# Performance work log

Hardware: AMD Instinct MI355X
Metric: run time of the kernel (lower is better)

The kernel has to match this reference:

```python
import jax, jax.numpy as jnp
import numpy as np

DIM = 128
DIM_HEAD = 32
HEADS = 4
EPS = 1e-12  # F.normalize eps


def _l2_normalize(t, axis=-1):
    # matches torch F.normalize(p=2): x / max(||x||, eps)
    n = jnp.sqrt(jnp.sum(t * t, axis=axis, keepdims=True))
    return t / jnp.maximum(n, EPS)


def _dwconv3x3(x_nhwc, k_hwio, c):
    # depthwise 3x3, stride 1, SAME padding, no bias
    return jax.lax.conv_general_dilated(
        x_nhwc, k_hwio, window_strides=(1, 1), padding='SAME',
        dimension_numbers=('NHWC', 'HWIO', 'NHWC'), feature_group_count=c)


def setup_inputs() -> dict:
    key = jax.random.key(0)
    ks = jax.random.split(key, 10)
    b, h, w = 4, 256, 256
    inner = DIM_HEAD * HEADS  # == DIM
    s = 0.02
    return {
        'x': jax.random.normal(ks[0], (b, h, w, DIM), jnp.float32),
        'illumination_feature': jax.random.uniform(ks[1], (b, h, w, inner), jnp.float32),
        'Wq': jax.random.normal(ks[2], (DIM, inner), jnp.float32) * s,  # stored (in,out)
        'Wk': jax.random.normal(ks[3], (DIM, inner), jnp.float32) * s,
        'Wv': jax.random.normal(ks[4], (DIM, inner), jnp.float32) * s,
        'rescale': jnp.ones((HEADS, 1, 1), jnp.float32),
        'Wp': jax.random.normal(ks[5], (inner, DIM), jnp.float32) * s,
        'bp': jnp.zeros((DIM,), jnp.float32),
        'pe_w1': jax.random.normal(ks[6], (3, 3, 1, DIM), jnp.float32) * s,  # HWIO depthwise
        'pe_w2': jax.random.normal(ks[7], (3, 3, 1, DIM), jnp.float32) * s,
    }


def reference(x, illumination_feature, Wq, Wk, Wv, rescale, Wp, bp, pe_w1, pe_w2):
    b, h, w, c = x.shape
    n = h * w
    heads = rescale.shape[0]
    xf = x.reshape(b, n, c)
    ilf = illumination_feature.reshape(b, n, -1)

    q_inp = xf @ Wq  # [b,n,heads*d]
    k_inp = xf @ Wk
    v_inp = xf @ Wv

    def to_heads(t):  # b n (h d) -> b h n d
        return t.reshape(b, n, heads, -1).transpose(0, 2, 1, 3)

    q = to_heads(q_inp)
    k = to_heads(k_inp)
    v = to_heads(v_inp) * to_heads(ilf)  # illumination gating

    # transpose to channel attention layout: b h d n
    q = q.transpose(0, 1, 3, 2)
    k = k.transpose(0, 1, 3, 2)
    v = v.transpose(0, 1, 3, 2)

    q = _l2_normalize(q, axis=-1)
    k = _l2_normalize(k, axis=-1)

    attn = jnp.einsum('bhdn,bhen->bhde', k, q) * rescale  # [b,h,d,d]
    attn = jax.nn.softmax(attn, axis=-1)
    out = jnp.einsum('bhde,bhen->bhdn', attn, v)  # [b,h,d,n]

    # b h d n -> b n (h d)
    out = out.transpose(0, 3, 1, 2).reshape(b, n, -1)
    x1 = (out @ Wp + bp).reshape(b, h, w, c)

    # positional branch: depthwise conv -> GELU -> depthwise conv on v_inp (NHWC)
    v_img = v_inp.reshape(b, h, w, -1)
    x2 = _dwconv3x3(v_img, pe_w1, c)
    x2 = jax.nn.gelu(x2, approximate=False)
    x2 = _dwconv3x3(x2, pe_w2, c)

    return x1 + x2
```

## Files before the change

### kernel.cpp

```cpp
#include <hip/hip_runtime.h>
#include <math.h>

#define B_ 4
#define C_ 128
#define H_ 256
#define W_ 256
#define NPIX (H_*W_)
#define HEADS_ 4

typedef unsigned int uint;
typedef unsigned short ushort;
typedef __attribute__((ext_vector_type(8))) __bf16 bf16x8;
typedef __attribute__((ext_vector_type(4))) float f32x4;

__device__ __forceinline__ ushort f2bf(float f){
    uint u = __builtin_bit_cast(uint, f);
    u += 0x7FFFu + ((u>>16)&1u);
    return (ushort)(u>>16);
}
__device__ __forceinline__ float bf2f(ushort h){
    uint u = ((uint)h)<<16;
    return __builtin_bit_cast(float, u);
}
__device__ __forceinline__ __bf16 f2bfv(float f){
    return __builtin_bit_cast(__bf16, f2bf(f));
}
__device__ __forceinline__ int swz3(int i){ return (i ^ (i>>3)) & 7; }

__global__ __launch_bounds__(512) void k12(const float* __restrict__ x, const float* __restrict__ Wv,
                                           float* __restrict__ S, ushort* __restrict__ vinp){
    __shared__ __align__(16) char smX[32768];
    __shared__ __align__(16) char smT[32768];
    int blk = blockIdx.x;
    int b = blk >> 7, chunk = blk & 127;
    long base = ((long)b*NPIX + (long)chunk*512) * C_;
    int t = threadIdx.x, lane = t & 63, w = t >> 6;
    int wm = w >> 2, wn = w & 3;
    int m0 = wm*64, n0 = wn*32;

    bf16x8 Bv[4][2];
    #pragma unroll
    for(int kk=0;kk<4;kk++){
        int kb = kk*32 + (lane>>4)*8;
        #pragma unroll
        for(int j=0;j<2;j++){
            int col = n0 + j*16 + (lane&15);
            bf16x8 v;
            #pragma unroll
            for(int jj=0;jj<8;jj++) v[jj] = f2bfv(Wv[(kb+jj)*C_ + col]);
            Bv[kk][j] = v;
        }
    }

    f32x4 acc_s[4][2];
    #pragma unroll
    for(int i=0;i<4;i++)
        #pragma unroll
        for(int j=0;j<2;j++) acc_s[i][j] = {0.f,0.f,0.f,0.f};

    for(int tile=0; tile<4; ++tile){
        {
            int rp = (t>>5)*2;
            int c0 = (t&31)*4;
            const float* xp = x + base + (long)tile*128*C_;
            #pragma unroll
            for(int p=0;p<4;p++){
                int r = p*32 + rp;
                float4 a0 = *(const float4*)(xp + r*C_ + c0);
                float4 a1 = *(const float4*)(xp + (r+1)*C_ + c0);
                ushort h0[4] = {f2bf(a0.x), f2bf(a0.y), f2bf(a0.z), f2bf(a0.w)};
                ushort h1[4] = {f2bf(a1.x), f2bf(a1.y), f2bf(a1.z), f2bf(a1.w)};
                uint2 pk0, pk1;
                pk0.x = (uint)h0[0] | ((uint)h0[1]<<16);
                pk0.y = (uint)h0[2] | ((uint)h0[3]<<16);
                pk1.x = (uint)h1[0] | ((uint)h1[1]<<16);
                pk1.y = (uint)h1[2] | ((uint)h1[3]<<16);
                *(uint2*)(smX + r*256     + ((2*c0) ^ (swz3(r)<<4)))   = pk0;
                *(uint2*)(smX + (r+1)*256 + ((2*c0) ^ (swz3(r+1)<<4))) = pk1;
                #pragma unroll
                for(int i=0;i<4;i++){
                    int ch = c0+i;
                    uint pk = (uint)h0[i] | ((uint)h1[i]<<16);
                    *(uint*)(smT + ch*256 + ((2*r) ^ (swz3(ch)<<4))) = pk;
                }
            }
        }
        __syncthreads();

        f32x4 acc_v[4][2];
        #pragma unroll
        for(int i=0;i<4;i++)
            #pragma unroll
            for(int j=0;j<2;j++) acc_v[i][j] = {0.f,0.f,0.f,0.f};

        #pragma unroll
        for(int kk=0;kk<4;kk++){
            int kb = kk*32 + (lane>>4)*8;
            bf16x8 A[4];
            #pragma unroll
            for(int i=0;i<4;i++){
                int r = m0 + i*16 + (lane&15);
                A[i] = *(const bf16x8*)(smX + r*256 + ((2*kb) ^ (swz3(r)<<4)));
            }
            #pragma unroll
            for(int i=0;i<4;i++)
                #pragma unroll
                for(int j=0;j<2;j++)
                    acc_v[i][j] = __builtin_amdgcn_mfma_f32_16x16x32_bf16(A[i], Bv[kk][j], acc_v[i][j], 0,0,0);
            bf16x8 As[4], Bs[2];
            #pragma unroll
            for(int i=0;i<4;i++){
                int ch = m0 + i*16 + (lane&15);
                As[i] = *(const bf16x8*)(smT + ch*256 + ((2*kb) ^ (swz3(ch)<<4)));
            }
            #pragma unroll
            for(int j=0;j<2;j++){
                int ch = n0 + j*16 + (lane&15);
                Bs[j] = *(const bf16x8*)(smT + ch*256 + ((2*kb) ^ (swz3(ch)<<4)));
            }
            #pragma unroll
            for(int i=0;i<4;i++)
                #pragma unroll
                for(int j=0;j<2;j++)
                    acc_s[i][j] = __builtin_amdgcn_mfma_f32_16x16x32_bf16(As[i], Bs[j], acc_s[i][j], 0,0,0);
        }
        __syncthreads();
        {
            int rq = (lane>>4)*4, cc = lane&15;
            #pragma unroll
            for(int i=0;i<4;i++)
                #pragma unroll
                for(int j=0;j<2;j++)
                    #pragma unroll
                    for(int rg=0;rg<4;rg++){
                        int row = m0 + i*16 + rq + rg;
                        int col = n0 + j*16 + cc;
                        *(ushort*)(smX + row*256 + ((2*col) ^ (swz3(row)<<4))) = f2bf(acc_v[i][j][rg]);
                    }
        }
        __syncthreads();
        {
            long off = base + (long)tile*128*C_;
            #pragma unroll
            for(int p=0;p<4;p++){
                int idx = p*512 + t;
                int row = idx >> 4, ub = idx & 15;
                uint4 d = *(const uint4*)(smX + row*256 + ((ub*16) ^ (swz3(row)<<4)));
                *(uint4*)(vinp + off + row*C_ + ub*8) = d;
            }
        }
        __syncthreads();
    }
    float* Sb = S + b*C_*C_;
    int rq = (lane>>4)*4, cc = lane&15;
    #pragma unroll
    for(int i=0;i<4;i++)
        #pragma unroll
        for(int j=0;j<2;j++)
            #pragma unroll
            for(int rg=0;rg<4;rg++){
                int row = m0 + i*16 + rq + rg;
                int col = n0 + j*16 + cc;
                atomicAdd(&Sb[row*C_ + col], acc_s[i][j][rg]);
            }
}

__global__ __launch_bounds__(256) void k3a(const float* __restrict__ S, const float* __restrict__ Wq,
                                           const float* __restrict__ Wk, float* __restrict__ TQ,
                                           float* __restrict__ nrm){
    int b = blockIdx.x >> 7, c = blockIdx.x & 127;
    __shared__ float sS[C_];
    int t = threadIdx.x;
    if(t < C_) sS[t] = S[(b*C_+c)*C_ + t];
    __syncthreads();
    const float* Wm = (t < C_) ? Wq : Wk;
    int col = t & (C_-1);
    float acc = 0.f;
    #pragma unroll 4
    for(int c2=0;c2<C_;c2++) acc += sS[c2] * Wm[c2*C_ + col];
    if(t < C_){
        TQ[(b*C_+c)*C_ + col] = acc;
        atomicAdd(&nrm[b*256 + col], Wq[c*C_+col]*acc);
    } else {
        atomicAdd(&nrm[b*256 + C_ + col], Wk[c*C_+col]*acc);
    }
}

__global__ __launch_bounds__(256) void k3b(const float* __restrict__ TQ, const float* __restrict__ Wk,
                                           const float* __restrict__ rescale, const float* __restrict__ Wp,
                                           const float* __restrict__ nrm, ushort* __restrict__ WeffT){
    int b = blockIdx.x >> 2, h = blockIdx.x & 3;
    int t = threadIdx.x;
    __shared__ float sTQ[C_*32];
    __shared__ float sWk[C_*32];
    __shared__ float sG[32*32];
    __shared__ float sinq[32], sink[32];

    #pragma unroll
    for(int p=0;p<16;p++){
        int idx = p*256 + t;
        int c = idx >> 5, e = idx & 31;
        sTQ[idx] = TQ[(b*C_+c)*C_ + h*32 + e];
        sWk[idx] = Wk[c*C_ + h*32 + e];
    }
    if(t < 32) sinq[t] = 1.f/fmaxf(sqrtf(fmaxf(nrm[b*256 + h*32 + t], 0.f)), 1e-12f);
    else if(t < 64) sink[t-32] = 1.f/fmaxf(sqrtf(fmaxf(nrm[b*256 + C_ + h*32 + (t-32)], 0.f)), 1e-12f);
    __syncthreads();

    float g[4];
    #pragma unroll
    for(int p=0;p<4;p++){
        int idx = p*256 + t;
        int d = idx >> 5, e = idx & 31;
        float a = 0.f;
        #pragma unroll 4
        for(int c=0;c<C_;c++) a += sWk[c*32+d]*sTQ[c*32+e];
        g[p] = a;
    }
    #pragma unroll
    for(int p=0;p<4;p++) sG[p*256 + t] = g[p];
    __syncthreads();

    if(t < 32){
        int d = t;
        float rs = rescale[h] * sink[d];
        float l[32]; float mx = -1e30f;
        #pragma unroll
        for(int e=0;e<32;e++){ l[e] = sG[d*32+e]*rs*sinq[e]; mx = fmaxf(mx, l[e]); }
        float sum = 0.f;
        #pragma unroll
        for(int e=0;e<32;e++){ l[e] = expf(l[e]-mx); sum += l[e]; }
        float inv = 1.f/sum;
        #pragma unroll
        for(int e=0;e<32;e++) sG[d*32+e] = l[e]*inv;
    }
    __syncthreads();

    #pragma unroll
    for(int p=0;p<16;p++){
        int idx = p*256 + t;
        int d = idx >> 7, c = idx & 127;
        sTQ[idx] = Wp[(h*32+d)*C_ + c];
    }
    __syncthreads();

    #pragma unroll
    for(int p=0;p<16;p++){
        int idx = p*256 + t;
        int c = idx >> 5, e = idx & 31;
        float a = 0.f;
        #pragma unroll
        for(int d=0;d<32;d++) a += sG[d*32+e]*sTQ[d*128+c];
        WeffT[((long)b*C_+c)*C_ + h*32 + e] = f2bf(a);
    }
}

__global__ __launch_bounds__(256) void k4a_conv1(const ushort* __restrict__ vinp, const float* __restrict__ w1,
                                                 ushort* __restrict__ c1){
    int blk0 = blockIdx.x;
    int blk = (blk0 & 7)*128 + (blk0 >> 3);
    int b = blk >> 8; int y = blk & 255;
    int t = threadIdx.x;
    int c0 = (t & 15)*8;
    int pg = t >> 4;
    float wreg[9][8];
    #pragma unroll
    for(int k=0;k<9;k++){
        float4 a = *(const float4*)(w1 + k*C_ + c0);
        float4 bq = *(const float4*)(w1 + k*C_ + c0 + 4);
        wreg[k][0]=a.x; wreg[k][1]=a.y; wreg[k][2]=a.z; wreg[k][3]=a.w;
        wreg[k][4]=bq.x; wreg[k][5]=bq.y; wreg[k][6]=bq.z; wreg[k][7]=bq.w;
    }
    const ushort* vb = vinp + (long)b*NPIX*C_;
    ushort* cb = c1 + (long)b*NPIX*C_;

    float colA[3][8], colB[3][8], colC[3][8];
    int xbase = pg*16;

    auto loadcol = [&](float (*col)[8], int xcol){
        #pragma unroll
        for(int ky=0;ky<3;ky++){
            int yy = y + ky - 1;
            if(xcol>=0 && xcol<W_ && yy>=0 && yy<H_){
                uint4 vv = *(const uint4*)(vb + ((long)yy*W_ + xcol)*C_ + c0);
                const ushort* pv = (const ushort*)&vv;
                #pragma unroll
                for(int i=0;i<8;i++) col[ky][i] = bf2f(pv[i]);
            } else {
                #pragma unroll
                for(int i=0;i<8;i++) col[ky][i] = 0.f;
            }
        }
    };
    loadcol(colA, xbase-1);
    loadcol(colB, xbase);
    #pragma unroll
    for(int q=0;q<16;q++){
        int xx = xbase + q;
        loadcol(colC, xx+1);
        float s[8];
        #pragma unroll
        for(int i=0;i<8;i++){
            float a = 0.f;
            #pragma unroll
            for(int ky=0;ky<3;ky++){
                a += colA[ky][i]*wreg[ky*3+0][i];
                a += colB[ky][i]*wreg[ky*3+1][i];
                a += colC[ky][i]*wreg[ky*3+2][i];
            }
            s[i] = a;
        }
        uint op[4];
        #pragma unroll
        for(int i2=0;i2<4;i2++){
            float va = s[i2*2],   ga = 0.5f*va*(1.0f+erff(va*0.70710678118654752f));
            float vb2 = s[i2*2+1], gb = 0.5f*vb2*(1.0f+erff(vb2*0.70710678118654752f));
            op[i2] = (uint)f2bf(ga) | ((uint)f2bf(gb)<<16);
        }
        uint4 o; o.x=op[0]; o.y=op[1]; o.z=op[2]; o.w=op[3];
        *(uint4*)(cb + ((long)y*W_ + xx)*C_ + c0) = o;
        #pragma unroll
        for(int ky=0;ky<3;ky++)
            #pragma unroll
            for(int i=0;i<8;i++){ colA[ky][i]=colB[ky][i]; colB[ky][i]=colC[ky][i]; }
    }
}

__global__ __launch_bounds__(512) void k4bc(const ushort* __restrict__ vinp, const float* __restrict__ ilf,
                                            const ushort* __restrict__ WeffT, const float* __restrict__ bp,
                                            const ushort* __restrict__ c1, const float* __restrict__ w2,
                                            float* __restrict__ out){
    __shared__ __align__(16) char smem[65536];
    char* smv = smem;
    char* smo = smem;

    int blk0 = blockIdx.x;
    int blk = (blk0 & 7)*256 + (blk0 >> 3);
    int b = blk >> 9; int tileI = blk & 511;
    long rowbase = (long)b*NPIX + (long)tileI*128;
    int t = threadIdx.x, lane = t&63, w = t>>6;
    int wm = w>>2, wn = w&3;
    int m0 = wm*64, n0 = wn*32;

    bf16x8 Bw[4][2];
    {
        const ushort* wp = WeffT + b*C_*C_;
        #pragma unroll
        for(int kk=0;kk<4;kk++){
            int kb = kk*32 + (lane>>4)*8;
            #pragma unroll
            for(int j=0;j<2;j++){
                int col = n0 + j*16 + (lane&15);
                Bw[kk][j] = *(const bf16x8*)(wp + col*C_ + kb);
            }
        }
    }
    {
        const ushort* vp = vinp + rowbase*C_;
        const float*  ip = ilf + rowbase*C_;
        #pragma unroll
        for(int p=0;p<4;p++){
            int idx = p*512 + t;
            int r = idx >> 4;
            int cl = (idx & 15)*8;
            uint4 vv = *(const uint4*)(vp + r*C_ + cl);
            const ushort* pv = (const ushort*)&vv;
            float4 i0 = *(const float4*)(ip + r*C_ + cl);
            float4 i1 = *(const float4*)(ip + r*C_ + cl + 4);
            uint4 pk;
            pk.x = (uint)f2bf(bf2f(pv[0])*i0.x) | ((uint)f2bf(bf2f(pv[1])*i0.y)<<16);
            pk.y = (uint)f2bf(bf2f(pv[2])*i0.z) | ((uint)f2bf(bf2f(pv[3])*i0.w)<<16);
            pk.z = (uint)f2bf(bf2f(pv[4])*i1.x) | ((uint)f2bf(bf2f(pv[5])*i1.y)<<16);
            pk.w = (uint)f2bf(bf2f(pv[6])*i1.z) | ((uint)f2bf(bf2f(pv[7])*i1.w)<<16);
            *(uint4*)(smv + r*256 + ((2*cl) ^ (swz3(r)<<4))) = pk;
        }
    }
    __syncthreads();

    f32x4 acc[4][2];
    #pragma unroll
    for(int i=0;i<4;i++)
        #pragma unroll
        for(int j=0;j<2;j++) acc[i][j] = {0.f,0.f,0.f,0.f};

    #pragma unroll
    for(int kk=0;kk<4;kk++){
        int kb = kk*32 + (lane>>4)*8;
        bf16x8 A[4];
        #pragma unroll
        for(int i=0;i<4;i++){
            int r = m0 + i*16 + (lane&15);
            A[i] = *(const bf16x8*)(smv + r*256 + ((2*kb) ^ (swz3(r)<<4)));
        }
        #pragma unroll
        for(int i=0;i<4;i++)
            #pragma unroll
            for(int j=0;j<2;j++)
                acc[i][j] = __builtin_amdgcn_mfma_f32_16x16x32_bf16(A[i], Bw[kk][j], acc[i][j], 0,0,0);
    }
    __syncthreads();
    {
        int rq = (lane>>4)*4, cc = lane&15;
        #pragma unroll
        for(int i=0;i<4;i++)
            #pragma unroll
            for(int j=0;j<2;j++)
                #pragma unroll
                for(int rg=0;rg<4;rg++){
                    int row = m0 + i*16 + rq + rg;
                    int col = n0 + j*16 + cc;
                    *(float*)(smo + row*512 + ((col*4) ^ (swz3(row)<<4))) = acc[i][j][rg];
                }
    }
    __syncthreads();

    int yt = tileI >> 1;
    int x0 = (tileI & 1) << 7;
    int c0 = (t & 15)*8;
    int pg = t >> 4;
    float wreg[9][8];
    #pragma unroll
    for(int k=0;k<9;k++){
        float4 a = *(const float4*)(w2 + k*C_ + c0);
        float4 bq = *(const float4*)(w2 + k*C_ + c0 + 4);
        wreg[k][0]=a.x; wreg[k][1]=a.y; wreg[k][2]=a.z; wreg[k][3]=a.w;
        wreg[k][4]=bq.x; wreg[k][5]=bq.y; wreg[k][6]=bq.z; wreg[k][7]=bq.w;
    }
    float bias[8];
    {
        float4 b0 = *(const float4*)(bp + c0);
        float4 b1 = *(const float4*)(bp + c0 + 4);
        bias[0]=b0.x; bias[1]=b0.y; bias[2]=b0.z; bias[3]=b0.w;
        bias[4]=b1.x; bias[5]=b1.y; bias[6]=b1.z; bias[7]=b1.w;
    }
    const ushort* cb = c1 + (long)b*NPIX*C_;
    float* ob = out + ((long)b*NPIX + (long)yt*W_)*C_;

    float colA[3][8], colB[3][8], colC[3][8];
    int xbase = x0 + pg*4;

    auto loadcol = [&](float (*col)[8], int xcol){
        #pragma unroll
        for(int ky=0;ky<3;ky++){
            int yy = yt + ky - 1;
            if(xcol>=0 && xcol<W_ && yy>=0 && yy<H_){
                uint4 vv = *(const uint4*)(cb + ((long)yy*W_ + xcol)*C_ + c0);
                const ushort* pv = (const ushort*)&vv;
                #pragma unroll
                for(int i=0;i<8;i++) col[ky][i] = bf2f(pv[i]);
            } else {
                #pragma unroll
                for(int i=0;i<8;i++) col[ky][i] = 0.f;
            }
        }
    };
    loadcol(colA, xbase-1);
    loadcol(colB, xbase);
    #pragma unroll
    for(int q=0;q<4;q++){
        int xx = xbase + q;
        int r  = pg*4 + q;
        loadcol(colC, xx+1);
        float s[8];
        #pragma unroll
        for(int i=0;i<8;i++){
            float a = 0.f;
            #pragma unroll
            for(int ky=0;ky<3;ky++){
                a += colA[ky][i]*wreg[ky*3+0][i];
                a += colB[ky][i]*wreg[ky*3+1][i];
                a += colC[ky][i]*wreg[ky*3+2][i];
            }
            s[i] = a;
        }
        float4 m0v = *(const float4*)(smo + r*512 + (((c0  )*4) ^ (swz3(r)<<4)));
        float4 m1v = *(const float4*)(smo + r*512 + (((c0+4)*4) ^ (swz3(r)<<4)));
        float4 o0, o1;
        o0.x = m0v.x + bias[0] + s[0];
        o0.y = m0v.y + bias[1] + s[1];
        o0.z = m0v.z + bias[2] + s[2];
        o0.w = m0v.w + bias[3] + s[3];
        o1.x = m1v.x + bias[4] + s[4];
        o1.y = m1v.y + bias[5] + s[5];
        o1.z = m1v.z + bias[6] + s[6];
        o1.w = m1v.w + bias[7] + s[7];
        float* op2 = ob + (long)xx*C_ + c0;
        *(float4*)(op2)     = o0;
        *(float4*)(op2 + 4) = o1;
        #pragma unroll
        for(int ky=0;ky<3;ky++)
            #pragma unroll
            for(int i=0;i<8;i++){ colA[ky][i]=colB[ky][i]; colB[ky][i]=colC[ky][i]; }
    }
}

extern "C" void kernel_launch(void* const* d_in, const int* in_sizes, int n_in,
                              void* d_out, int out_size, void* d_ws, size_t ws_size,
                              hipStream_t stream){
    (void)in_sizes; (void)n_in; (void)out_size; (void)ws_size;
    const float* x    = (const float*)d_in[0];
    const float* ilf  = (const float*)d_in[1];
    const float* Wq   = (const float*)d_in[2];
    const float* Wk   = (const float*)d_in[3];
    const float* Wv   = (const float*)d_in[4];
    const float* rsc  = (const float*)d_in[5];
    const float* Wp   = (const float*)d_in[6];
    const float* bp   = (const float*)d_in[7];
    const float* w1   = (const float*)d_in[8];
    const float* w2   = (const float*)d_in[9];
    float* out = (float*)d_out;
    char* ws = (char*)d_ws;

    ushort* vinp  = (ushort*)ws;
    ushort* c1    = (ushort*)(ws + 67108864);
    float*  TQ    = (float*)(ws + 67108864);
    float*  S     = (float*)(ws + 134217728);
    float*  nrm   = (float*)(ws + 134479872);
    ushort* WeffT = (ushort*)(ws + 134483968);

    hipMemsetAsync(S, 0, 262144 + 4096, stream);
    hipLaunchKernelGGL(k12,      dim3(512),  dim3(512), 0, stream, x, Wv, S, vinp);
    hipLaunchKernelGGL(k3a,      dim3(512),  dim3(256), 0, stream, S, Wq, Wk, TQ, nrm);
    hipLaunchKernelGGL(k3b,      dim3(16),   dim3(256), 0, stream, TQ, Wk, rsc, Wp, nrm, WeffT);
    hipLaunchKernelGGL(k4a_conv1,dim3(1024), dim3(256), 0, stream, vinp, w1, c1);
    hipLaunchKernelGGL(k4bc,     dim3(2048), dim3(512), 0, stream, vinp, ilf, WeffT, bp, c1, w2, out);
}
```

Baseline: 309.8 us.

## Halve conv1 rows per block and restructure k4bc to 256 threads with LDS weights

conv1 now splits each image row into two blocks (2048 blocks, 8 pixels per thread) for more parallelism. k4bc drops from 512 to 256 threads: the per-batch projection weights are staged into swizzled shared memory instead of held in registers, each wave computes a 64x64 MFMA tile, and each thread handles 8 pixels in the conv2 epilogue. The output staging buffer loses its swizzle and becomes plain row-major, which may add LDS bank conflicts and extra scalar LDS reads. The aim is to cut redundant global weight reads and raise per-thread work, at the cost of fewer threads per block and more registers.

After: 279.7 us. -9.7%, faster.

```diff
diff --git a/kernel.cpp b/kernel.cpp
--- a/kernel.cpp
+++ b/kernel.cpp
@@ -258,8 +258,8 @@
 __global__ __launch_bounds__(256) void k4a_conv1(const ushort* __restrict__ vinp, const float* __restrict__ w1,
                                                  ushort* __restrict__ c1){
     int blk0 = blockIdx.x;
-    int blk = (blk0 & 7)*128 + (blk0 >> 3);
-    int b = blk >> 8; int y = blk & 255;
+    int blk = (blk0 & 7)*256 + (blk0 >> 3);
+    int b = blk >> 9; int y = (blk >> 1) & 255; int xh = blk & 1;
     int t = threadIdx.x;
     int c0 = (t & 15)*8;
     int pg = t >> 4;
@@ -275,7 +275,7 @@
     ushort* cb = c1 + (long)b*NPIX*C_;
 
     float colA[3][8], colB[3][8], colC[3][8];
-    int xbase = pg*16;
+    int xbase = xh*128 + pg*8;
 
     auto loadcol = [&](float (*col)[8], int xcol){
         #pragma unroll
@@ -295,7 +295,7 @@
     loadcol(colA, xbase-1);
     loadcol(colB, xbase);
     #pragma unroll
-    for(int q=0;q<16;q++){
+    for(int q=0;q<8;q++){
         int xx = xbase + q;
         loadcol(colC, xx+1);
         float s[8];
@@ -326,43 +326,38 @@
     }
 }
 
-__global__ __launch_bounds__(512) void k4bc(const ushort* __restrict__ vinp, const float* __restrict__ ilf,
+__global__ __launch_bounds__(256) void k4bc(const ushort* __restrict__ vinp, const float* __restrict__ ilf,
                                             const ushort* __restrict__ WeffT, const float* __restrict__ bp,
                                             const ushort* __restrict__ c1, const float* __restrict__ w2,
                                             float* __restrict__ out){
     __shared__ __align__(16) char smem[65536];
     char* smv = smem;
-    char* smo = smem;
+    char* smw = smem + 32768;
+    float* smo = (float*)smem;
 
     int blk0 = blockIdx.x;
     int blk = (blk0 & 7)*256 + (blk0 >> 3);
     int b = blk >> 9; int tileI = blk & 511;
     long rowbase = (long)b*NPIX + (long)tileI*128;
-    int t = threadIdx.x, lane = t&63, w = t>>6;
-    int wm = w>>2, wn = w&3;
-    int m0 = wm*64, n0 = wn*32;
-
-    bf16x8 Bw[4][2];
+    int t = threadIdx.x, lane=t&63, w=t>>6;
+    int m0=(w>>1)*64, n0=(w&1)*64;
     {
         const ushort* wp = WeffT + b*C_*C_;
         #pragma unroll
-        for(int kk=0;kk<4;kk++){
-            int kb = kk*32 + (lane>>4)*8;
-            #pragma unroll
-            for(int j=0;j<2;j++){
-                int col = n0 + j*16 + (lane&15);
-                Bw[kk][j] = *(const bf16x8*)(wp + col*C_ + kb);
-            }
+        for(int p=0;p<8;p++){
+            int idx = p*256 + t;
+            int cR = idx >> 4; int ub = idx & 15;
+            uint4 d = *(const uint4*)(wp + cR*C_ + ub*8);
+            *(uint4*)(smw + cR*256 + ((ub*16) ^ (swz3(cR)<<4))) = d;
         }
     }
     {
         const ushort* vp = vinp + rowbase*C_;
         const float*  ip = ilf + rowbase*C_;
         #pragma unroll
-        for(int p=0;p<4;p++){
-            int idx = p*512 + t;
-            int r = idx >> 4;
-            int cl = (idx & 15)*8;
+        for(int p=0;p<8;p++){
+            int r = p*16 + (t>>4);
+            int cl = (t&15)*8;
             uint4 vv = *(const uint4*)(vp + r*C_ + cl);
             const ushort* pv = (const ushort*)&vv;
             float4 i0 = *(const float4*)(ip + r*C_ + cl);
@@ -377,40 +372,46 @@
     }
     __syncthreads();
 
-    f32x4 acc[4][2];
+    f32x4 acc[4][4];
     #pragma unroll
     for(int i=0;i<4;i++)
         #pragma unroll
-        for(int j=0;j<2;j++) acc[i][j] = {0.f,0.f,0.f,0.f};
+        for(int j=0;j<4;j++) acc[i][j] = {0.f,0.f,0.f,0.f};
 
     #pragma unroll
     for(int kk=0;kk<4;kk++){
         int kb = kk*32 + (lane>>4)*8;
-        bf16x8 A[4];
+        bf16x8 A[4], Bf[4];
         #pragma unroll
         for(int i=0;i<4;i++){
             int r = m0 + i*16 + (lane&15);
             A[i] = *(const bf16x8*)(smv + r*256 + ((2*kb) ^ (swz3(r)<<4)));
         }
         #pragma unroll
+        for(int j=0;j<4;j++){
+            int o = n0 + j*16 + (lane&15);
+            Bf[j] = *(const bf16x8*)(smw + o*256 + ((2*kb) ^ (swz3(o)<<4)));
+        }
+        #pragma unroll
         for(int i=0;i<4;i++)
             #pragma unroll
-            for(int j=0;j<2;j++)
-                acc[i][j] = __builtin_amdgcn_mfma_f32_16x16x32_bf16(A[i], Bw[kk][j], acc[i][j], 0,0,0);
+            for(int j=0;j<4;j++)
+                acc[i][j] = __builtin_amdgcn_mfma_f32_16x16x32_bf16(A[i], Bf[j], acc[i][j], 0,0,0);
     }
     __syncthreads();
     {
         int rq = (lane>>4)*4, cc = lane&15;
         #pragma unroll
-        for(int i=0;i<4;i++)
-            #pragma unroll
-            for(int j=0;j<2;j++)
+        for(int j=0;j<4;j++){
+            int col = n0 + j*16 + cc;
+            #pragma unroll
+            for(int i=0;i<4;i++)
                 #pragma unroll
                 for(int rg=0;rg<4;rg++){
                     int row = m0 + i*16 + rq + rg;
-                    int col = n0 + j*16 + cc;
-                    *(float*)(smo + row*512 + ((col*4) ^ (swz3(row)<<4))) = acc[i][j][rg];
+                    smo[row*C_ + col] = acc[i][j][rg];
                 }
+        }
     }
     __syncthreads();
 
@@ -437,7 +438,7 @@
     float* ob = out + ((long)b*NPIX + (long)yt*W_)*C_;
 
     float colA[3][8], colB[3][8], colC[3][8];
-    int xbase = x0 + pg*4;
+    int xbase = x0 + pg*8;
 
     auto loadcol = [&](float (*col)[8], int xcol){
         #pragma unroll
@@ -457,9 +458,9 @@
     loadcol(colA, xbase-1);
     loadcol(colB, xbase);
     #pragma unroll
-    for(int q=0;q<4;q++){
+    for(int q=0;q<8;q++){
         int xx = xbase + q;
-        int r  = pg*4 + q;
+        int r  = pg*8 + q;
         loadcol(colC, xx+1);
         float s[8];
         #pragma unroll
@@ -473,17 +474,15 @@
             }
             s[i] = a;
         }
-        float4 m0v = *(const float4*)(smo + r*512 + (((c0  )*4) ^ (swz3(r)<<4)));
-        float4 m1v = *(const float4*)(smo + r*512 + (((c0+4)*4) ^ (swz3(r)<<4)));
         float4 o0, o1;
-        o0.x = m0v.x + bias[0] + s[0];
-        o0.y = m0v.y + bias[1] + s[1];
-        o0.z = m0v.z + bias[2] + s[2];
-        o0.w = m0v.w + bias[3] + s[3];
-        o1.x = m1v.x + bias[4] + s[4];
-        o1.y = m1v.y + bias[5] + s[5];
-        o1.z = m1v.z + bias[6] + s[6];
-        o1.w = m1v.w + bias[7] + s[7];
+        o0.x = smo[r*C_ + c0 + 0] + bias[0] + s[0];
+        o0.y = smo[r*C_ + c0 + 1] + bias[1] + s[1];
+        o0.z = smo[r*C_ + c0 + 2] + bias[2] + s[2];
+        o0.w = smo[r*C_ + c0 + 3] + bias[3] + s[3];
+        o1.x = smo[r*C_ + c0 + 4] + bias[4] + s[4];
+        o1.y = smo[r*C_ + c0 + 5] + bias[5] + s[5];
+        o1.z = smo[r*C_ + c0 + 6] + bias[6] + s[6];
+        o1.w = smo[r*C_ + c0 + 7] + bias[7] + s[7];
         float* op2 = ob + (long)xx*C_ + c0;
         *(float4*)(op2)     = o0;
         *(float4*)(op2 + 4) = o1;
@@ -522,6 +521,6 @@
     hipLaunchKernelGGL(k12,      dim3(512),  dim3(512), 0, stream, x, Wv, S, vinp);
     hipLaunchKernelGGL(k3a,      dim3(512),  dim3(256), 0, stream, S, Wq, Wk, TQ, nrm);
     hipLaunchKernelGGL(k3b,      dim3(16),   dim3(256), 0, stream, TQ, Wk, rsc, Wp, nrm, WeffT);
-    hipLaunchKernelGGL(k4a_conv1,dim3(1024), dim3(256), 0, stream, vinp, w1, c1);
-    hipLaunchKernelGGL(k4bc,     dim3(2048), dim3(512), 0, stream, vinp, ilf, WeffT, bp, c1, w2, out);
-}
+    hipLaunchKernelGGL(k4a_conv1,dim3(2048), dim3(256), 0, stream, vinp, w1, c1);
+    hipLaunchKernelGGL(k4bc,     dim3(2048), dim3(256), 0, stream, vinp, ilf, WeffT, bp, c1, w2, out);
+}
```
